# Performance work log

Measured on AMD Instinct MI355X. Metric: run time of the kernel, lower is better.

Reference implementation:

```python
import jax, jax.numpy as jnp
import numpy as np

B, L, D = 8, 2048, 512

def setup_inputs() -> dict:
    key = jax.random.key(0)
    ks = jax.random.split(key, 10)
    s = 1.0 / np.sqrt(D)
    inp = {
        "raw_data_inputs": jax.random.normal(ks[0], (B, L, D), jnp.float32),
        "handcraft_data_inputs": jax.random.normal(ks[1], (B, L, D), jnp.float32),
    }
    names = ["Wq_r", "Wk_r", "Wv_r", "Wq_h", "Wk_h", "Wv_h"]
    for i, n in enumerate(names):
        inp[n] = jax.random.normal(ks[2 + i], (D, D), jnp.float32) * s
        inp["b" + n[1:]] = jnp.zeros((D,), jnp.float32)
    return inp

def reference(raw_data_inputs, handcraft_data_inputs,
              Wq_r, bq_r, Wk_r, bk_r, Wv_r, bv_r,
              Wq_h, bq_h, Wk_h, bk_h, Wv_h, bv_h):
    # Six Dense projections (no head split, no 1/sqrt(d) scaling, no mask)
    Qr = raw_data_inputs @ Wq_r + bq_r            # [B, L, D]
    Kr = raw_data_inputs @ Wk_r + bk_r
    Vr = raw_data_inputs @ Wv_r + bv_r
    Qh = handcraft_data_inputs @ Wq_h + bq_h
    Kh = handcraft_data_inputs @ Wk_h + bk_h
    Vh = handcraft_data_inputs @ Wv_h + bv_h
    # raw queries attend to handcraft keys, but aggregate raw values
    Ar = jax.nn.softmax(jnp.einsum("bqd,bkd->bqk", Qr, Kh), axis=-1)  # [B, L, L]
    context_raw = jnp.einsum("bqk,bkd->bqd", Ar, Vr)
    # handcraft queries attend to raw keys, aggregate handcraft values
    Ah = jax.nn.softmax(jnp.einsum("bqd,bkd->bqk", Qh, Kr), axis=-1)
    context_hand = jnp.einsum("bqk,bkd->bqd", Ah, Vh)
    return (context_raw, context_hand)
```

## Files before the change

### kernel.cpp

```cpp
#include <hip/hip_runtime.h>

typedef unsigned short u16;
typedef _Float16 f16;
typedef __attribute__((ext_vector_type(8))) f16 f16x8;
typedef __attribute__((ext_vector_type(4))) float fx4;
typedef __attribute__((ext_vector_type(8))) u16 u16x8;
typedef __attribute__((ext_vector_type(4))) u16 u16x4;

#define SZE 8388608u

__device__ __forceinline__ u16 f2h_bits(float x) {
  union { f16 h; u16 u; } v; v.h = (f16)x; return v.u;
}

__device__ __forceinline__ void gl2lds16(const void* g, void* l) {
  __builtin_amdgcn_global_load_lds(
      (const __attribute__((address_space(1))) unsigned int*)g,
      (__attribute__((address_space(3))) unsigned int*)l, 16, 0, 0);
}

template <int C>
__device__ __forceinline__ float dppf(float x) {
  return __int_as_float(__builtin_amdgcn_update_dpp(
      __float_as_int(x), __float_as_int(x), C, 0xf, 0xf, false));
}
__device__ __forceinline__ float rowmax16(float x) {
  x = fmaxf(x, dppf<0xB1>(x));
  x = fmaxf(x, dppf<0x4E>(x));
  x = fmaxf(x, dppf<0x141>(x));
  x = fmaxf(x, dppf<0x140>(x));
  return x;
}
__device__ __forceinline__ float rowsum16(float x) {
  x += dppf<0xB1>(x);
  x += dppf<0x4E>(x);
  x += dppf<0x141>(x);
  x += dppf<0x140>(x);
  return x;
}

__global__ __launch_bounds__(256) void convert_x(const float* __restrict__ x0,
                                                 const float* __restrict__ x1,
                                                 u16* __restrict__ xh) {
  size_t i = ((size_t)blockIdx.x * 256 + threadIdx.x) * 8;
  const float* src = (i < SZE) ? (x0 + i) : (x1 + (i - SZE));
  float4 a = *(const float4*)(src);
  float4 b = *(const float4*)(src + 4);
  u16x8 o;
  o[0] = f2h_bits(a.x); o[1] = f2h_bits(a.y);
  o[2] = f2h_bits(a.z); o[3] = f2h_bits(a.w);
  o[4] = f2h_bits(b.x); o[5] = f2h_bits(b.y);
  o[6] = f2h_bits(b.z); o[7] = f2h_bits(b.w);
  *(u16x8*)(xh + i) = o;
}

__global__ __launch_bounds__(256) void wtrans(
    const float* __restrict__ w0, const float* __restrict__ w1,
    const float* __restrict__ w2, const float* __restrict__ w3,
    const float* __restrict__ w4, const float* __restrict__ w5,
    u16* __restrict__ wt) {
  __shared__ float tile[32][33];
  const int z = blockIdx.z;
  const float* W = z == 0 ? w0 : z == 1 ? w1 : z == 2 ? w2
                 : z == 3 ? w3 : z == 4 ? w4 : w5;
  u16* WT = wt + (size_t)z * 262144u;
  const int k0 = blockIdx.x * 32, n0 = blockIdx.y * 32;
  const int tx = threadIdx.x, ty = threadIdx.y;
  for (int j = 0; j < 32; j += 8)
    tile[ty + j][tx] = W[(size_t)(k0 + ty + j) * 512 + n0 + tx];
  __syncthreads();
  for (int j = 0; j < 32; j += 8)
    WT[(size_t)(n0 + ty + j) * 512 + k0 + tx] = f2h_bits(tile[tx][ty + j]);
}

__global__ __launch_bounds__(256, 3) void proj_gemm(
    const u16* __restrict__ xh, const u16* __restrict__ wt,
    u16* __restrict__ qkv,
    const float* __restrict__ b0, const float* __restrict__ b1,
    const float* __restrict__ b2, const float* __restrict__ b3,
    const float* __restrict__ b4, const float* __restrict__ b5) {
  const int proj = blockIdx.z;
  const u16* X = xh + (proj < 3 ? 0u : SZE);
  const u16* W = wt + (size_t)proj * 262144u;
  u16* out = qkv + (size_t)proj * SZE;
  const float* bias = proj == 0 ? b0 : proj == 1 ? b1 : proj == 2 ? b2
                    : proj == 3 ? b3 : proj == 4 ? b4 : b5;
  const int m0 = blockIdx.x * 128, n0 = blockIdx.y * 128;
  const int t = threadIdx.x, lane = t & 63, w = t >> 6;
  const int wr = w >> 1, wc = w & 1, ml = lane & 15, q = lane >> 4;
  __shared__ u16 smem[16384];
  u16* sAb[2] = {smem, smem + 4096};
  u16* sBb[2] = {smem + 8192, smem + 12288};
  fx4 acc[4][4] = {};
  for (int r = 0; r < 2; ++r) {
    int ci = r * 256 + t;
    int row = ci >> 2, kc = ci & 3;
    gl2lds16(X + (size_t)(m0 + row) * 512 + kc * 8, sAb[0] + ci * 8);
    gl2lds16(W + (size_t)(n0 + row) * 512 + kc * 8, sBb[0] + ci * 8);
  }
  __syncthreads();
  for (int kt = 0; kt < 16; ++kt) {
    const int c = kt & 1;
    if (kt < 15) {
      const int k0 = (kt + 1) * 32;
      for (int r = 0; r < 2; ++r) {
        int ci = r * 256 + t;
        int row = ci >> 2, kc = ci & 3;
        gl2lds16(X + (size_t)(m0 + row) * 512 + (k0 + kc * 8), sAb[c ^ 1] + ci * 8);
        gl2lds16(W + (size_t)(n0 + row) * 512 + (k0 + kc * 8), sBb[c ^ 1] + ci * 8);
      }
    }
    f16x8 af[4], bf[4];
    for (int i = 0; i < 4; ++i) {
      af[i] = *(const f16x8*)(sAb[c] + ((wr * 64 + i * 16 + ml) * 4 + q) * 8);
      bf[i] = *(const f16x8*)(sBb[c] + ((wc * 64 + i * 16 + ml) * 4 + q) * 8);
    }
    for (int i = 0; i < 4; ++i)
      for (int j = 0; j < 4; ++j)
        acc[i][j] = __builtin_amdgcn_mfma_f32_16x16x32_f16(af[i], bf[j],
                                                           acc[i][j], 0, 0, 0);
    __syncthreads();
  }
  const int pm = proj % 3;
  if (pm == 2) {
    for (int j = 0; j < 4; ++j) {
      const int n = n0 + wc * 64 + j * 16 + ml;
      const float bv = bias[n];
      for (int i = 0; i < 4; ++i) {
        const int mb = m0 + wr * 64 + i * 16 + q * 4;
        const int l = mb & 2047;
        size_t a = (size_t)(mb >> 11) * 1048576u + (size_t)(l >> 5) * 16384u
                 + (size_t)(((l & 31) >> 3) * 512 + n) * 8u + (size_t)(l & 7);
        u16x4 pk;
        for (int r = 0; r < 4; ++r) pk[r] = f2h_bits(acc[i][j][r] + bv);
        *(u16x4*)(out + a) = pk;
      }
    }
  } else {
    if (pm == 0) {
      for (int j = 0; j < 4; ++j) {
        const float bv = bias[n0 + wc * 64 + j * 16 + ml];
        for (int i = 0; i < 4; ++i) {
          const int lm = wr * 64 + i * 16 + q * 4;
          const int ln = wc * 64 + j * 16 + ml;
          for (int r = 0; r < 4; ++r)
            smem[(lm + r) * 128 + ln] = f2h_bits(acc[i][j][r] + bv);
        }
      }
    } else {
      for (int j = 0; j < 4; ++j) {
        const float bv = bias[n0 + wc * 64 + j * 16 + ml];
        for (int i = 0; i < 4; ++i) {
          const int kt2 = wr * 2 + (i >> 1);
          const int key5 = (i & 1) * 16 + q * 4;
          const int dcl = wc * 8 + j * 2 + (ml >> 3);
          const int d8 = ml & 7;
          u16* cb = smem + kt2 * 4096 + dcl * 256 + d8;
          for (int r = 0; r < 4; ++r)
            cb[(key5 + r) * 8] = f2h_bits(acc[i][j][r] + bv);
        }
      }
    }
    __syncthreads();
    if (pm == 0) {
      for (int s = 0; s < 8; ++s) {
        int ci = s * 256 + t;
        int row = ci >> 4, c8 = ci & 15;
        *(u16x8*)(out + (size_t)(m0 + row) * 512 + n0 + c8 * 8) =
            *(const u16x8*)(smem + ci * 8);
      }
    } else {
      const size_t bbase = (size_t)(m0 >> 11) * 1048576u +
                           (size_t)((m0 & 2047) >> 5) * 16384u +
                           (size_t)(n0 >> 3) * 256u;
      for (int s = 0; s < 8; ++s) {
        int ci = s * 256 + t;
        int kt2 = ci >> 9, inner = ci & 511;
        *(u16x8*)(out + bbase + (size_t)kt2 * 16384u + inner * 8) =
            *(const u16x8*)(smem + ci * 8);
      }
    }
  }
}

__global__ __launch_bounds__(512, 2) void attn_kernel(const u16* __restrict__ qkv,
                                                      float* __restrict__ out) {
  const int t = threadIdx.x, lane = t & 63, w = t >> 6;
  const int ml = lane & 15, q = lane >> 4;
  const int n = blockIdx.x;
  const int xcd = n & 7, slot = n >> 3;
  const int g = xcd * 2 + (slot >> 4);
  const int qt = slot & 15;
  const int b = g >> 1, tt = g & 1;

  const u16* Q  = qkv + (tt ? (size_t)3 * SZE : (size_t)0);
  const u16* K  = qkv + (tt ? (size_t)1 * SZE : (size_t)4 * SZE);
  const u16* Vt = qkv + (tt ? (size_t)5 * SZE : (size_t)2 * SZE);
  float* O = out + (tt ? (size_t)SZE : (size_t)0) +
             ((size_t)b * 2048 + qt * 128) * 512;
  const u16* Qb = Q + ((size_t)b * 2048 + qt * 128) * 512;
  const u16* Kb = K + (size_t)b * 1048576u;
  const u16* Vb = Vt + (size_t)b * 1048576u;

  __shared__ u16 sK[2][16384];
  __shared__ u16 sV[2][16384];
  __shared__ u16 sP[8 * 640];

  f16x8 qf[16];
  {
    const u16* qrow = Qb + (size_t)(w * 16 + ml) * 512 + q * 8;
#pragma unroll
    for (int ks = 0; ks < 16; ++ks) qf[ks] = *(const f16x8*)(qrow + ks * 32);
  }

  fx4 acc[32] = {};
  fx4 mrun = {-3.0e38f, -3.0e38f, -3.0e38f, -3.0e38f};
  fx4 lrun = {0.f, 0.f, 0.f, 0.f};
  u16* wp = sP + w * 640;

#pragma unroll
  for (int r = 0; r < 4; ++r) {
    int p = r * 512 + t;
    gl2lds16(Kb + (size_t)p * 8, sK[0] + p * 8);
    gl2lds16(Vb + (size_t)p * 8, sV[0] + p * 8);
  }
  __syncthreads();

  for (int it = 0; it < 64; ++it) {
    const int c = it & 1;
    const u16* sKc = sK[c];
    const u16* sVc = sV[c];
    if (it < 63) {
      const u16* Kn = Kb + (size_t)(it + 1) * 16384u;
      const u16* Vn = Vb + (size_t)(it + 1) * 16384u;
#pragma unroll
      for (int r = 0; r < 4; ++r) {
        int p = r * 512 + t;
        gl2lds16(Kn + (size_t)p * 8, sK[c ^ 1] + p * 8);
        gl2lds16(Vn + (size_t)p * 8, sV[c ^ 1] + p * 8);
      }
    }
    fx4 s0 = {0.f, 0.f, 0.f, 0.f}, s1 = {0.f, 0.f, 0.f, 0.f};
    __builtin_amdgcn_s_setprio(1);
#pragma unroll
    for (int ks = 0; ks < 16; ++ks) {
      f16x8 kf0 = *(const f16x8*)(sKc + ((ks * 4 + q) * 32 + ml) * 8);
      f16x8 kf1 = *(const f16x8*)(sKc + ((ks * 4 + q) * 32 + 16 + ml) * 8);
      s0 = __builtin_amdgcn_mfma_f32_16x16x32_f16(qf[ks], kf0, s0, 0, 0, 0);
      s1 = __builtin_amdgcn_mfma_f32_16x16x32_f16(qf[ks], kf1, s1, 0, 0, 0);
    }
    __builtin_amdgcn_s_setprio(0);
    fx4 mx, alpha, p0, p1, sm;
#pragma unroll
    for (int r = 0; r < 4; ++r) mx[r] = rowmax16(fmaxf(s0[r], s1[r]));
    bool need = false;
#pragma unroll
    for (int r = 0; r < 4; ++r) {
      float mn = fmaxf(mrun[r], mx[r]);
      alpha[r] = __expf(mrun[r] - mn);
      mrun[r] = mn;
      p0[r] = __expf(s0[r] - mn);
      p1[r] = __expf(s1[r] - mn);
      need |= (alpha[r] != 1.0f);
    }
#pragma unroll
    for (int r = 0; r < 4; ++r) sm[r] = rowsum16(p0[r] + p1[r]);
#pragma unroll
    for (int r = 0; r < 4; ++r) lrun[r] = alpha[r] * lrun[r] + sm[r];
#pragma unroll
    for (int r = 0; r < 4; ++r) {
      wp[(q * 4 + r) * 40 + ml] = f2h_bits(p0[r]);
      wp[(q * 4 + r) * 40 + 16 + ml] = f2h_bits(p1[r]);
    }
    if (__any(need)) {
#pragma unroll
      for (int nj = 0; nj < 32; ++nj) {
        acc[nj][0] *= alpha[0]; acc[nj][1] *= alpha[1];
        acc[nj][2] *= alpha[2]; acc[nj][3] *= alpha[3];
      }
    }
    f16x8 pf = *(const f16x8*)(wp + ml * 40 + q * 8);
    __builtin_amdgcn_s_setprio(1);
#pragma unroll
    for (int nj = 0; nj < 32; ++nj) {
      f16x8 vf = *(const f16x8*)(sVc + (q * 512 + nj * 16 + ml) * 8);
      acc[nj] = __builtin_amdgcn_mfma_f32_16x16x32_f16(pf, vf, acc[nj], 0, 0, 0);
    }
    __builtin_amdgcn_s_setprio(0);
    __syncthreads();
  }
  fx4 linv;
#pragma unroll
  for (int r = 0; r < 4; ++r) linv[r] = 1.0f / lrun[r];
  float* Ob = O + (size_t)(w * 16 + q * 4) * 512 + ml;
#pragma unroll
  for (int nj = 0; nj < 32; ++nj) {
#pragma unroll
    for (int r = 0; r < 4; ++r)
      Ob[(size_t)r * 512 + nj * 16] = acc[nj][r] * linv[r];
  }
}

extern "C" void kernel_launch(void* const* d_in, const int* in_sizes, int n_in,
                              void* d_out, int out_size, void* d_ws, size_t ws_size,
                              hipStream_t stream) {
  u16* ws = (u16*)d_ws;
  u16* xh = ws;
  u16* wt = ws + 16777216u;
  u16* qkv = ws + 18350080u;

  convert_x<<<8192, 256, 0, stream>>>((const float*)d_in[0],
                                      (const float*)d_in[1], xh);
  wtrans<<<dim3(16, 16, 6), dim3(32, 8), 0, stream>>>(
      (const float*)d_in[2], (const float*)d_in[4], (const float*)d_in[6],
      (const float*)d_in[8], (const float*)d_in[10], (const float*)d_in[12], wt);
  proj_gemm<<<dim3(128, 4, 6), 256, 0, stream>>>(
      xh, wt, qkv,
      (const float*)d_in[3], (const float*)d_in[5], (const float*)d_in[7],
      (const float*)d_in[9], (const float*)d_in[11], (const float*)d_in[13]);
  attn_kernel<<<256, 512, 0, stream>>>(qkv, (float*)d_out);
}
```

Before: 394.3 us.

## Triple-buffer projection GEMM loads with explicit vmcnt waits

Switches the projection GEMM from double to triple buffering in LDS, prefetching two K-tiles ahead. It replaces the per-iteration __syncthreads with explicit s_waitcnt vmcnt counts and raw barriers, so only the current stage's loads must finish. The aim is to hide more global-load latency behind MFMA work. The cost is 48KB of LDS per block instead of 32KB, which may reduce occupancy under launch_bounds(256,3).

```diff
diff --git a/kernel.cpp b/kernel.cpp
--- a/kernel.cpp
+++ b/kernel.cpp
@@ -88,38 +88,49 @@
   const int m0 = blockIdx.x * 128, n0 = blockIdx.y * 128;
   const int t = threadIdx.x, lane = t & 63, w = t >> 6;
   const int wr = w >> 1, wc = w & 1, ml = lane & 15, q = lane >> 4;
-  __shared__ u16 smem[16384];
-  u16* sAb[2] = {smem, smem + 4096};
-  u16* sBb[2] = {smem + 8192, smem + 12288};
+  __shared__ u16 smem[24576];
   fx4 acc[4][4] = {};
-  for (int r = 0; r < 2; ++r) {
-    int ci = r * 256 + t;
-    int row = ci >> 2, kc = ci & 3;
-    gl2lds16(X + (size_t)(m0 + row) * 512 + kc * 8, sAb[0] + ci * 8);
-    gl2lds16(W + (size_t)(n0 + row) * 512 + kc * 8, sBb[0] + ci * 8);
-  }
-  __syncthreads();
+  for (int pk = 0; pk < 2; ++pk) {
+    for (int r = 0; r < 2; ++r) {
+      int ci = r * 256 + t;
+      int row = ci >> 2, kc = ci & 3;
+      gl2lds16(X + (size_t)(m0 + row) * 512 + (pk * 32 + kc * 8),
+               smem + pk * 4096 + ci * 8);
+      gl2lds16(W + (size_t)(n0 + row) * 512 + (pk * 32 + kc * 8),
+               smem + 12288 + pk * 4096 + ci * 8);
+    }
+  }
   for (int kt = 0; kt < 16; ++kt) {
-    const int c = kt & 1;
-    if (kt < 15) {
-      const int k0 = (kt + 1) * 32;
+    const int cur = kt % 3;
+    if (kt < 14) {
+      const int stg = (kt + 2) % 3;
+      const int k0 = (kt + 2) * 32;
       for (int r = 0; r < 2; ++r) {
         int ci = r * 256 + t;
         int row = ci >> 2, kc = ci & 3;
-        gl2lds16(X + (size_t)(m0 + row) * 512 + (k0 + kc * 8), sAb[c ^ 1] + ci * 8);
-        gl2lds16(W + (size_t)(n0 + row) * 512 + (k0 + kc * 8), sBb[c ^ 1] + ci * 8);
-      }
-    }
+        gl2lds16(X + (size_t)(m0 + row) * 512 + (k0 + kc * 8),
+                 smem + stg * 4096 + ci * 8);
+        gl2lds16(W + (size_t)(n0 + row) * 512 + (k0 + kc * 8),
+                 smem + 12288 + stg * 4096 + ci * 8);
+      }
+    }
+    if (kt < 14)      asm volatile("s_waitcnt vmcnt(8)" ::: "memory");
+    else if (kt == 14) asm volatile("s_waitcnt vmcnt(4)" ::: "memory");
+    else               asm volatile("s_waitcnt vmcnt(0)" ::: "memory");
+    __builtin_amdgcn_s_barrier();
+    const u16* sAc = smem + cur * 4096;
+    const u16* sBc = smem + 12288 + cur * 4096;
     f16x8 af[4], bf[4];
     for (int i = 0; i < 4; ++i) {
-      af[i] = *(const f16x8*)(sAb[c] + ((wr * 64 + i * 16 + ml) * 4 + q) * 8);
-      bf[i] = *(const f16x8*)(sBb[c] + ((wc * 64 + i * 16 + ml) * 4 + q) * 8);
+      af[i] = *(const f16x8*)(sAc + ((wr * 64 + i * 16 + ml) * 4 + q) * 8);
+      bf[i] = *(const f16x8*)(sBc + ((wc * 64 + i * 16 + ml) * 4 + q) * 8);
     }
     for (int i = 0; i < 4; ++i)
       for (int j = 0; j < 4; ++j)
         acc[i][j] = __builtin_amdgcn_mfma_f32_16x16x32_f16(af[i], bf[j],
                                                            acc[i][j], 0, 0, 0);
-    __syncthreads();
+    asm volatile("s_waitcnt lgkmcnt(0)" ::: "memory");
+    __builtin_amdgcn_s_barrier();
   }
   const int pm = proj % 3;
   if (pm == 2) {
```

Result: no change. 395.2 us (+0.2%).
